# Kernel tuning notes

Hardware: AMD Instinct MI355X
Metric: run time of the kernel (lower is better)

## Reference

```python
import jax, jax.numpy as jnp
import numpy as np

SIZE = (128.0, 128.0, 128.0)
FEATURE_BLOCK_IDS = (1, 2, 3)


def _trilerp(feat, coords, power):
    # feat: [B, D, H, W, C]; coords: [B, N, 3] in [0, 1]
    B = coords.shape[0]
    scale = jnp.asarray([0.5 ** power * SIZE[0],
                         0.5 ** power * SIZE[1],
                         0.5 ** power * SIZE[2]], dtype=coords.dtype)
    hi = float(min(feat.shape[1:4])) - 1.01
    idx = jnp.clip(coords * scale, 0.01, hi)  # [B, N, 3]
    ix, iy, iz = idx[..., 0], idx[..., 1], idx[..., 2]
    x1, x2 = jnp.floor(ix), jnp.ceil(ix)
    y1, y2 = jnp.floor(iy), jnp.ceil(iy)
    z1, z2 = jnp.floor(iz), jnp.ceil(iz)
    b = jnp.arange(B)[:, None]  # broadcast batch index

    def g(xi, yi, zi):
        return feat[b, xi.astype(jnp.int32), yi.astype(jnp.int32), zi.astype(jnp.int32)]

    wx, wx2 = (ix - x1)[..., None], (x2 - ix)[..., None]
    wy, wy2 = (iy - y1)[..., None], (y2 - iy)[..., None]
    wz, wz2 = (iz - z1)[..., None], (z2 - iz)[..., None]

    # z = z1 plane
    lerp_x1 = g(x2, y1, z1) * wx + g(x1, y1, z1) * wx2
    lerp_x2 = g(x2, y2, z1) * wx + g(x1, y2, z1) * wx2
    lerp_y1 = lerp_x2 * wy + lerp_x1 * wy2
    # z = z2 plane
    lerp_x1 = g(x2, y1, z2) * wx + g(x1, y1, z2) * wx2
    lerp_x2 = g(x2, y2, z2) * wx + g(x1, y2, z2) * wx2
    lerp_y2 = lerp_x2 * wy + lerp_x1 * wy2
    return lerp_y2 * wz + lerp_y1 * wz2  # [B, N, C]


def setup_inputs() -> dict:
    key = jax.random.key(0)
    ks = jax.random.split(key, 7)
    B, N = 2, 50000
    return {
        'features0': jax.random.normal(ks[0], (B, 128, 128, 128, 1), jnp.float32),
        'features1': jax.random.normal(ks[1], (B, 64, 64, 64, 32), jnp.float32),
        'features2': jax.random.normal(ks[2], (B, 32, 32, 32, 64), jnp.float32),
        'features3': jax.random.normal(ks[3], (B, 16, 16, 16, 128), jnp.float32),
        'features4': jax.random.normal(ks[4], (B, 8, 8, 8, 256), jnp.float32),
        'mesh_coords': jax.random.uniform(ks[5], (B, N, 3), jnp.float32),
        'mesh_features': jax.random.normal(ks[6], (B, N, 3), jnp.float32),
    }


def reference(features0, features1, features2, features3, features4, mesh_coords, mesh_features):
    feats = [features0, features1, features2, features3, features4]
    # mesh_coords is [B, N, 3] -> one coord group, reshape is identity
    sampled = [_trilerp(feats[i], mesh_coords, i) for i in FEATURE_BLOCK_IDS]
    out = jnp.concatenate(sampled, axis=-1)
    return jnp.concatenate([out, mesh_features], axis=-1)
```

## Files before the change

### kernel.cpp

```cpp
#include <hip/hip_runtime.h>


#define BUCK_AXIS 8
#define BUCK_PER_BATCH 512
#define MAX_BUCKETS 1024

__device__ __forceinline__ int point_batch(int p, int N) {
    int b = 0;
    while (p >= N) { p -= N; ++b; }
    return b;
}

__device__ __forceinline__ int bucket_key(const float* __restrict__ coords,
                                          int t, int N) {
    const float cx = coords[t * 3 + 0];
    const float cy = coords[t * 3 + 1];
    const float cz = coords[t * 3 + 2];
    int kx = (int)(cx * (float)BUCK_AXIS);
    int ky = (int)(cy * (float)BUCK_AXIS);
    int kz = (int)(cz * (float)BUCK_AXIS);
    kx = min(max(kx, 0), BUCK_AXIS - 1);
    ky = min(max(ky, 0), BUCK_AXIS - 1);
    kz = min(max(kz, 0), BUCK_AXIS - 1);
    const int b = point_batch(t, N);
    return b * BUCK_PER_BATCH + ((kx << 6) | (ky << 3) | kz);
}

__global__ void zero_kernel(int* __restrict__ hist, int n) {
    const int t = blockIdx.x * blockDim.x + threadIdx.x;
    if (t < n) hist[t] = 0;
}

__global__ void hist_kernel(const float* __restrict__ coords,
                            int* __restrict__ hist, int N, int P) {
    const int t = blockIdx.x * blockDim.x + threadIdx.x;
    if (t >= P) return;
    atomicAdd(&hist[bucket_key(coords, t, N)], 1);
}

__global__ __launch_bounds__(MAX_BUCKETS) void scan_kernel(
    const int* __restrict__ hist, int* __restrict__ ofs, int n) {
    __shared__ int tmp[MAX_BUCKETS];
    const int t = threadIdx.x;
    const int v = (t < n) ? hist[t] : 0;
    tmp[t] = v;
    __syncthreads();
    for (int s = 1; s < MAX_BUCKETS; s <<= 1) {
        const int add = (t >= s) ? tmp[t - s] : 0;
        __syncthreads();
        tmp[t] += add;
        __syncthreads();
    }
    if (t < n) ofs[t] = tmp[t] - v;
}

__global__ void scatter_kernel(const float* __restrict__ coords,
                               int* __restrict__ ofs, int* __restrict__ perm,
                               int N, int P) {
    const int t = blockIdx.x * blockDim.x + threadIdx.x;
    if (t >= P) return;
    const int key = bucket_key(coords, t, N);
    const int b   = key >= BUCK_PER_BATCH;
    const int idx = atomicAdd(&ofs[key], 1);
    perm[idx] = t | (b << 28);
}

__device__ __forceinline__ float4 lerpw(const float4 a, const float4 b,
                                        float w, float w2) {
    float4 r;
    r.x = a.x * w + b.x * w2;
    r.y = a.y * w + b.y * w2;
    r.z = a.z * w + b.z * w2;
    r.w = a.w * w + b.w * w2;
    return r;
}

__global__ __launch_bounds__(256) void trilerp_main(
    const float* __restrict__ f1,
    const float* __restrict__ f2,
    const float* __restrict__ f3,
    const float* __restrict__ coords,
    const float* __restrict__ meshf,
    float* __restrict__ out,
    const int* __restrict__ perm,
    int N, int P)
{
    const int lane = threadIdx.x & 63;
    const int w    = (blockIdx.x * 256 + threadIdx.x) >> 6;
    const int i0   = w * 2;
    if (i0 >= P) return;
    const bool has1 = (i0 + 1) < P;

    int pts[2], bs[2];
    if (perm) {
        const int e0 = perm[i0];
        const int e1 = has1 ? perm[i0 + 1] : e0;
        pts[0] = e0 & 0x0FFFFFFF;  bs[0] = e0 >> 28;
        pts[1] = e1 & 0x0FFFFFFF;  bs[1] = e1 >> 28;
    } else {
        pts[0] = i0;                       bs[0] = point_batch(pts[0], N);
        pts[1] = has1 ? (i0 + 1) : i0;     bs[1] = point_batch(pts[1], N);
    }

    if (lane >= 56) {
        const int i = lane - 56;
        if (i < 6) {
            const int pi = i / 3;
            const int ch = i - pi * 3;
            if (pi == 0 || has1) {
                const int p = pts[pi];
                __builtin_nontemporal_store(meshf[p * 3 + ch],
                                            &out[p * 227 + 224 + ch]);
            }
        }
        return;
    }

    const float4* fp; int D, C4, c4g, oc;
    if (lane < 8)       { fp = (const float4*)f1; D = 64; C4 = 8;  c4g = lane;      oc = lane * 4;             }
    else if (lane < 24) { fp = (const float4*)f2; D = 32; C4 = 16; c4g = lane - 8;  oc = 32 + (lane - 8) * 4;  }
    else                { fp = (const float4*)f3; D = 16; C4 = 32; c4g = lane - 24; oc = 96 + (lane - 24) * 4; }

    const float scale = (float)D;
    const float hi    = (float)((double)D - 1.01);
    const int   vol4  = D * D * D * C4;

    float4 v[2][8];
    float wxa[2], wxb[2], wya[2], wyb[2], wza[2], wzb[2];

    #pragma unroll
    for (int q = 0; q < 2; ++q) {
        const int p = pts[q];
        const float cx = coords[p * 3 + 0];
        const float cy = coords[p * 3 + 1];
        const float cz = coords[p * 3 + 2];

        const float ix = fminf(fmaxf(cx * scale, 0.01f), hi);
        const float iy = fminf(fmaxf(cy * scale, 0.01f), hi);
        const float iz = fminf(fmaxf(cz * scale, 0.01f), hi);

        const float x1f = floorf(ix), x2f = ceilf(ix);
        const float y1f = floorf(iy), y2f = ceilf(iy);
        const float z1f = floorf(iz), z2f = ceilf(iz);
        const int x1 = (int)x1f, x2 = (int)x2f;
        const int y1 = (int)y1f, y2 = (int)y2f;
        const int z1 = (int)z1f, z2 = (int)z2f;

        wxa[q] = ix - x1f; wxb[q] = x2f - ix;
        wya[q] = iy - y1f; wyb[q] = y2f - iy;
        wza[q] = iz - z1f; wzb[q] = z2f - iz;

        const int base4 = bs[q] * vol4 + c4g;
        #define IDX(X, Y, Z) (base4 + (((X) * D + (Y)) * D + (Z)) * C4)
        v[q][0] = fp[IDX(x1, y1, z1)];
        v[q][1] = fp[IDX(x2, y1, z1)];
        v[q][2] = fp[IDX(x1, y2, z1)];
        v[q][3] = fp[IDX(x2, y2, z1)];
        v[q][4] = fp[IDX(x1, y1, z2)];
        v[q][5] = fp[IDX(x2, y1, z2)];
        v[q][6] = fp[IDX(x1, y2, z2)];
        v[q][7] = fp[IDX(x2, y2, z2)];
        #undef IDX
    }

    #pragma unroll
    for (int q = 0; q < 2; ++q) {
        if (q == 1 && !has1) break;
        const float4 lx1a = lerpw(v[q][1], v[q][0], wxa[q], wxb[q]);
        const float4 lx2a = lerpw(v[q][3], v[q][2], wxa[q], wxb[q]);
        const float4 ly1  = lerpw(lx2a,    lx1a,    wya[q], wyb[q]);
        const float4 lx1b = lerpw(v[q][5], v[q][4], wxa[q], wxb[q]);
        const float4 lx2b = lerpw(v[q][7], v[q][6], wxa[q], wxb[q]);
        const float4 ly2  = lerpw(lx2b,    lx1b,    wya[q], wyb[q]);
        const float4 r    = lerpw(ly2,     ly1,     wza[q], wzb[q]);

        float* o = out + pts[q] * 227 + oc;
        __builtin_nontemporal_store(r.x, o + 0);
        __builtin_nontemporal_store(r.y, o + 1);
        __builtin_nontemporal_store(r.z, o + 2);
        __builtin_nontemporal_store(r.w, o + 3);
    }
}

extern "C" void kernel_launch(void* const* d_in, const int* in_sizes, int n_in,
                              void* d_out, int out_size, void* d_ws, size_t ws_size,
                              hipStream_t stream) {
    const float* f1     = (const float*)d_in[1];
    const float* f2     = (const float*)d_in[2];
    const float* f3     = (const float*)d_in[3];
    const float* coords = (const float*)d_in[5];
    const float* meshf  = (const float*)d_in[6];
    float* out = (float*)d_out;

    const int B = in_sizes[1] / (64 * 64 * 64 * 32);
    const int N = in_sizes[5] / (B * 3);
    const int P = B * N;

    int* hist = (int*)d_ws;
    int* ofs  = hist + MAX_BUCKETS;
    int* perm = hist + 2 * MAX_BUCKETS;
    const size_t need = (size_t)(2 * MAX_BUCKETS + P) * sizeof(int);
    const int nb = B * BUCK_PER_BATCH;
    const bool useSort = (ws_size >= need) && (nb <= MAX_BUCKETS);

    if (useSort) {
        zero_kernel<<<dim3((nb + 255) / 256), dim3(256), 0, stream>>>(hist, nb);
        hist_kernel<<<dim3((P + 255) / 256), dim3(256), 0, stream>>>(coords, hist, N, P);
        scan_kernel<<<dim3(1), dim3(MAX_BUCKETS), 0, stream>>>(hist, ofs, nb);
        scatter_kernel<<<dim3((P + 255) / 256), dim3(256), 0, stream>>>(coords, ofs, perm, N, P);
    }

    trilerp_main<<<dim3((P + 7) / 8), dim3(256), 0, stream>>>(
        f1, f2, f3, coords, meshf, out, useSort ? perm : nullptr, N, P);
}
```

Measured before the change: 252.6 us.

## Drop spatial bucket sort and issue all gathers before interpolation

Removes the four-kernel spatial bucketing pass (zero, histogram, scan, scatter), so the trilinear kernel now processes points in their original order. This drops the extra launches and the serialized single-block scan. The cost is the loss of gather locality for feature-volume accesses and of output-write locality. All sixteen gather indices are also computed first, then the loads are issued back to back behind a scheduling barrier to raise memory-level parallelism.

```diff
diff --git a/kernel.cpp b/kernel.cpp
--- a/kernel.cpp
+++ b/kernel.cpp
@@ -1,68 +1,10 @@
 #include <hip/hip_runtime.h>
 
-
-#define BUCK_AXIS 8
-#define BUCK_PER_BATCH 512
-#define MAX_BUCKETS 1024
 
 __device__ __forceinline__ int point_batch(int p, int N) {
     int b = 0;
     while (p >= N) { p -= N; ++b; }
     return b;
-}
-
-__device__ __forceinline__ int bucket_key(const float* __restrict__ coords,
-                                          int t, int N) {
-    const float cx = coords[t * 3 + 0];
-    const float cy = coords[t * 3 + 1];
-    const float cz = coords[t * 3 + 2];
-    int kx = (int)(cx * (float)BUCK_AXIS);
-    int ky = (int)(cy * (float)BUCK_AXIS);
-    int kz = (int)(cz * (float)BUCK_AXIS);
-    kx = min(max(kx, 0), BUCK_AXIS - 1);
-    ky = min(max(ky, 0), BUCK_AXIS - 1);
-    kz = min(max(kz, 0), BUCK_AXIS - 1);
-    const int b = point_batch(t, N);
-    return b * BUCK_PER_BATCH + ((kx << 6) | (ky << 3) | kz);
-}
-
-__global__ void zero_kernel(int* __restrict__ hist, int n) {
-    const int t = blockIdx.x * blockDim.x + threadIdx.x;
-    if (t < n) hist[t] = 0;
-}
-
-__global__ void hist_kernel(const float* __restrict__ coords,
-                            int* __restrict__ hist, int N, int P) {
-    const int t = blockIdx.x * blockDim.x + threadIdx.x;
-    if (t >= P) return;
-    atomicAdd(&hist[bucket_key(coords, t, N)], 1);
-}
-
-__global__ __launch_bounds__(MAX_BUCKETS) void scan_kernel(
-    const int* __restrict__ hist, int* __restrict__ ofs, int n) {
-    __shared__ int tmp[MAX_BUCKETS];
-    const int t = threadIdx.x;
-    const int v = (t < n) ? hist[t] : 0;
-    tmp[t] = v;
-    __syncthreads();
-    for (int s = 1; s < MAX_BUCKETS; s <<= 1) {
-        const int add = (t >= s) ? tmp[t - s] : 0;
-        __syncthreads();
-        tmp[t] += add;
-        __syncthreads();
-    }
-    if (t < n) ofs[t] = tmp[t] - v;
-}
-
-__global__ void scatter_kernel(const float* __restrict__ coords,
-                               int* __restrict__ ofs, int* __restrict__ perm,
-                               int N, int P) {
-    const int t = blockIdx.x * blockDim.x + threadIdx.x;
-    if (t >= P) return;
-    const int key = bucket_key(coords, t, N);
-    const int b   = key >= BUCK_PER_BATCH;
-    const int idx = atomicAdd(&ofs[key], 1);
-    perm[idx] = t | (b << 28);
 }
 
 __device__ __forceinline__ float4 lerpw(const float4 a, const float4 b,
@@ -75,37 +17,27 @@
     return r;
 }
 
-__global__ __launch_bounds__(256) void trilerp_main(
+__global__ __launch_bounds__(256) void trilerp_kernel(
     const float* __restrict__ f1,
     const float* __restrict__ f2,
     const float* __restrict__ f3,
     const float* __restrict__ coords,
     const float* __restrict__ meshf,
     float* __restrict__ out,
-    const int* __restrict__ perm,
     int N, int P)
 {
     const int lane = threadIdx.x & 63;
-    const int w    = (blockIdx.x * 256 + threadIdx.x) >> 6;
-    const int i0   = w * 2;
+    const int wv   = (blockIdx.x * 256 + threadIdx.x) >> 6;
+    const int i0   = wv * 2;
     if (i0 >= P) return;
     const bool has1 = (i0 + 1) < P;
 
-    int pts[2], bs[2];
-    if (perm) {
-        const int e0 = perm[i0];
-        const int e1 = has1 ? perm[i0 + 1] : e0;
-        pts[0] = e0 & 0x0FFFFFFF;  bs[0] = e0 >> 28;
-        pts[1] = e1 & 0x0FFFFFFF;  bs[1] = e1 >> 28;
-    } else {
-        pts[0] = i0;                       bs[0] = point_batch(pts[0], N);
-        pts[1] = has1 ? (i0 + 1) : i0;     bs[1] = point_batch(pts[1], N);
-    }
+    const int pts[2] = { i0, has1 ? (i0 + 1) : i0 };
 
     if (lane >= 56) {
         const int i = lane - 56;
         if (i < 6) {
-            const int pi = i / 3;
+            const int pi = i >= 3;
             const int ch = i - pi * 3;
             if (pi == 0 || has1) {
                 const int p = pts[pi];
@@ -125,7 +57,7 @@
     const float hi    = (float)((double)D - 1.01);
     const int   vol4  = D * D * D * C4;
 
-    float4 v[2][8];
+    int   idx[2][8];
     float wxa[2], wxb[2], wya[2], wyb[2], wza[2], wzb[2];
 
     #pragma unroll
@@ -150,18 +82,27 @@
         wya[q] = iy - y1f; wyb[q] = y2f - iy;
         wza[q] = iz - z1f; wzb[q] = z2f - iz;
 
-        const int base4 = bs[q] * vol4 + c4g;
+        const int base4 = point_batch(p, N) * vol4 + c4g;
         #define IDX(X, Y, Z) (base4 + (((X) * D + (Y)) * D + (Z)) * C4)
-        v[q][0] = fp[IDX(x1, y1, z1)];
-        v[q][1] = fp[IDX(x2, y1, z1)];
-        v[q][2] = fp[IDX(x1, y2, z1)];
-        v[q][3] = fp[IDX(x2, y2, z1)];
-        v[q][4] = fp[IDX(x1, y1, z2)];
-        v[q][5] = fp[IDX(x2, y1, z2)];
-        v[q][6] = fp[IDX(x1, y2, z2)];
-        v[q][7] = fp[IDX(x2, y2, z2)];
+        idx[q][0] = IDX(x1, y1, z1);
+        idx[q][1] = IDX(x2, y1, z1);
+        idx[q][2] = IDX(x1, y2, z1);
+        idx[q][3] = IDX(x2, y2, z1);
+        idx[q][4] = IDX(x1, y1, z2);
+        idx[q][5] = IDX(x2, y1, z2);
+        idx[q][6] = IDX(x1, y2, z2);
+        idx[q][7] = IDX(x2, y2, z2);
         #undef IDX
     }
+
+    float4 v[2][8];
+    #pragma unroll
+    for (int q = 0; q < 2; ++q)
+        #pragma unroll
+        for (int j = 0; j < 8; ++j)
+            v[q][j] = fp[idx[q][j]];
+
+    __builtin_amdgcn_sched_barrier(0);
 
     #pragma unroll
     for (int q = 0; q < 2; ++q) {
@@ -196,20 +137,6 @@
     const int N = in_sizes[5] / (B * 3);
     const int P = B * N;
 
-    int* hist = (int*)d_ws;
-    int* ofs  = hist + MAX_BUCKETS;
-    int* perm = hist + 2 * MAX_BUCKETS;
-    const size_t need = (size_t)(2 * MAX_BUCKETS + P) * sizeof(int);
-    const int nb = B * BUCK_PER_BATCH;
-    const bool useSort = (ws_size >= need) && (nb <= MAX_BUCKETS);
-
-    if (useSort) {
-        zero_kernel<<<dim3((nb + 255) / 256), dim3(256), 0, stream>>>(hist, nb);
-        hist_kernel<<<dim3((P + 255) / 256), dim3(256), 0, stream>>>(coords, hist, N, P);
-        scan_kernel<<<dim3(1), dim3(MAX_BUCKETS), 0, stream>>>(hist, ofs, nb);
-        scatter_kernel<<<dim3((P + 255) / 256), dim3(256), 0, stream>>>(coords, ofs, perm, N, P);
-    }
-
-    trilerp_main<<<dim3((P + 7) / 8), dim3(256), 0, stream>>>(
-        f1, f2, f3, coords, meshf, out, useSort ? perm : nullptr, N, P);
+    trilerp_kernel<<<dim3((P + 7) / 8), dim3(256), 0, stream>>>(
+        f1, f2, f3, coords, meshf, out, N, P);
 }
```

Measured after the change: 214.7 us. 15.0% less time.
